# Kernel optimization log

Hardware: AMD Instinct MI355X
Metric: run time of the kernel (lower is better)

## Reference

```python
import jax, jax.numpy as jnp
import numpy as np

BIT, ROW, COL = 4, 8, 8
Y_ROW, Z_COL, K = 128, 128, 256  # inter_dimension = 256, K8 = 32
K8 = K // 8
BATCH, SEQ = 8, 2048


def _unpack_bits(packed, n_bits):
    """Unpack uint8 along last axis, big-endian (MSB first), matching np.packbits."""
    shifts = jnp.arange(7, -1, -1, dtype=jnp.uint8)
    bits = (packed[..., None] >> shifts) & jnp.uint8(1)  # [..., k8, 8]
    return bits.reshape(*packed.shape[:-1], -1)[..., :n_bits]


def setup_inputs() -> dict:
    rng = np.random.default_rng(0)
    # Generate underlying binary tensors so Y_sum / Z_sum are consistent with packed bits.
    Yb = rng.integers(0, 2, size=(BIT, ROW, COL, Y_ROW, K), dtype=np.uint8)
    Zb = rng.integers(0, 2, size=(BIT, ROW, COL, K, Z_COL), dtype=np.uint8)
    Y_packed = np.packbits(Yb, axis=-1)                                # [BIT,ROW,COL,Y_ROW,K8]
    Z_packed = np.packbits(Zb.transpose(0, 1, 2, 4, 3), axis=-1)        # [BIT,ROW,COL,Z_COL,K8]
    Y_sum = Yb.sum(axis=-1, keepdims=True).astype(np.int32)             # [BIT,ROW,COL,Y_ROW,1]
    Z_sum = Zb.sum(axis=-2, keepdims=True).astype(np.int32)             # [BIT,ROW,COL,1,Z_COL]

    key = jax.random.key(0)
    k1, k2, k3, k4, k5, k6 = jax.random.split(key, 6)
    X = jax.random.normal(k1, (BATCH, SEQ, COL * Z_COL), dtype=jnp.float32)
    a = jax.random.normal(k2, (BIT, 1, 1, 1, 1), dtype=jnp.float32) * 0.1
    b = jax.random.normal(k3, (BIT, 1, 1, 1, 1), dtype=jnp.float32) * 0.1
    c = jax.random.normal(k4, (BIT, 1, 1, 1, 1), dtype=jnp.float32) * 0.1
    d = jax.random.normal(k5, (1, 1, 1, 1), dtype=jnp.float32) * 0.1
    bias = jax.random.normal(k6, (ROW * Y_ROW,), dtype=jnp.float32) * 0.1
    return {
        "X": X,
        "Y_packed": jnp.asarray(Y_packed),
        "Z_packed": jnp.asarray(Z_packed),
        "Y_sum": jnp.asarray(Y_sum),
        "Z_sum": jnp.asarray(Z_sum),
        "a": a, "b": b, "c": c, "d": d, "bias": bias,
    }


def reference(X, Y_packed, Z_packed, Y_sum, Z_sum, a, b, c, d, bias):
    dtype = X.dtype
    # Unpack bits (fallback path of _matmul_via_unpack) and do binary matmul.
    Y = _unpack_bits(Y_packed, K).astype(dtype)        # [BIT,ROW,COL,Y_ROW,K]
    Zt = _unpack_bits(Z_packed, K).astype(dtype)       # [BIT,ROW,COL,Z_COL,K]
    W_core = jnp.einsum('brcyk,brczk->brcyz', Y, Zt)   # [BIT,ROW,COL,Y_ROW,Z_COL]
    # Affine recombination over bit planes.
    W = a * W_core + b * Y_sum.astype(dtype) + c * Z_sum.astype(dtype)
    W = W.sum(axis=0) + d                               # [ROW,COL,Y_ROW,Z_COL]
    W = W.transpose(0, 2, 1, 3).reshape(ROW * Y_ROW, COL * Z_COL)
    return X @ W.T + bias
```

## Files before the change

kernel.cpp:

```cpp
#include <hip/hip_runtime.h>
#include <hip/hip_bf16.h>
#include <stdint.h>

typedef unsigned int u32;
typedef unsigned short u16;
typedef __attribute__((ext_vector_type(8))) short short8;
typedef __attribute__((ext_vector_type(4))) float floatx4;

#define N_DIM 1024
#define K_DIM 1024
#define M_DIM 16384
#define EPW  68

__device__ __forceinline__ u32 pack4(uint4 v) {
    return (v.x & 0xffu) | ((v.y & 0xffu) << 8) | ((v.z & 0xffu) << 16) | (v.w << 24);
}

__device__ __forceinline__ u16 bf16rne(float f) {
    u32 u = __float_as_uint(f);
    return (u16)((u + 0x7fffu + ((u >> 16) & 1u)) >> 16);
}

__device__ __forceinline__ void load16_lds(const void* g, void* l) {
    __builtin_amdgcn_global_load_lds(
        (const __attribute__((address_space(1))) void*)g,
        (__attribute__((address_space(3))) void*)l, 16, 0, 0);
}

__global__ __launch_bounds__(256) void build_w(
        const u32* __restrict__ yp, const u32* __restrict__ zp,
        const int* __restrict__ ysum, const int* __restrict__ zsum,
        const float* __restrict__ pa, const float* __restrict__ pb,
        const float* __restrict__ pc, const float* __restrict__ pd,
        __hip_bfloat16* __restrict__ Wb) {
    __shared__ u32 sY[4096];
    __shared__ u32 sZ[1024];
    __shared__ int sYs[512];
    __shared__ int sZs[128];

    const int tid = threadIdx.x;
    const int rc = blockIdx.x >> 2;
    const int zq = blockIdx.x & 3;
    const int r = rc >> 3, c = rc & 7;
    const int z0 = zq * 32;

    const uint4 d0 = ((const uint4*)yp)[0], d1 = ((const uint4*)yp)[1];
    const int sdet = __popc(d0.x) + __popc(d0.y) + __popc(d0.z) + __popc(d0.w)
                   + __popc(d1.x) + __popc(d1.y) + __popc(d1.z) + __popc(d1.w);
    const bool widened = (sdet != ysum[0]);

    if (!widened) {
#pragma unroll
        for (int j = 0; j < 4; ++j) {
            const int chunk = tid + j * 256;
            const int f = chunk * 4;
            const int bit = f >> 10, rem = f & 1023;
            const u32 gw = (u32)((bit * 64 + r * 8 + c) * 1024 + rem);
            ((uint4*)sY)[chunk] = *(const uint4*)(yp + gw);
        }
        {
            const int f = tid * 4;
            const int bit = f >> 8;
            const u32 gw = (u32)((bit * 64 + r * 8 + c) * 1024 + z0 * 8 + (f & 255));
            ((uint4*)sZ)[tid] = *(const uint4*)(zp + gw);
        }
    } else {
#pragma unroll
        for (int j = 0; j < 4; ++j) {
            const int chunk = tid + j * 256;
            const int f = chunk * 4;
            const int bit = f >> 10, rem = f & 1023;
            const u32 gw = (u32)((bit * 64 + r * 8 + c) * 1024 + rem);
            uint4 o;
            o.x = pack4(((const uint4*)yp)[gw + 0]);
            o.y = pack4(((const uint4*)yp)[gw + 1]);
            o.z = pack4(((const uint4*)yp)[gw + 2]);
            o.w = pack4(((const uint4*)yp)[gw + 3]);
            ((uint4*)sY)[chunk] = o;
        }
        {
            const int f = tid * 4;
            const int bit = f >> 8;
            const u32 gw = (u32)((bit * 64 + r * 8 + c) * 1024 + z0 * 8 + (f & 255));
            uint4 o;
            o.x = pack4(((const uint4*)zp)[gw + 0]);
            o.y = pack4(((const uint4*)zp)[gw + 1]);
            o.z = pack4(((const uint4*)zp)[gw + 2]);
            o.w = pack4(((const uint4*)zp)[gw + 3]);
            ((uint4*)sZ)[tid] = o;
        }
    }
    for (int j = tid; j < 512; j += 256) {
        const int bit = j >> 7, y = j & 127;
        sYs[j] = ysum[((bit * 8 + r) * 8 + c) * 128 + y];
    }
    if (tid < 128) {
        const int bit = tid >> 5, zl = tid & 31;
        sZs[tid] = zsum[((bit * 8 + r) * 8 + c) * 128 + z0 + zl];
    }
    __syncthreads();

    float av[4], bv[4], cv[4];
#pragma unroll
    for (int bit = 0; bit < 4; ++bit) { av[bit] = pa[bit]; bv[bit] = pb[bit]; cv[bit] = pc[bit]; }
    const float dv = pd[0];

    const int y = tid & 127;
    const int zh = tid >> 7;

    u32 yw[4][8];
    float base = dv;
#pragma unroll
    for (int bit = 0; bit < 4; ++bit) {
        const uint4 q0 = ((const uint4*)sY)[bit * 256 + y * 2];
        const uint4 q1 = ((const uint4*)sY)[bit * 256 + y * 2 + 1];
        yw[bit][0] = q0.x; yw[bit][1] = q0.y; yw[bit][2] = q0.z; yw[bit][3] = q0.w;
        yw[bit][4] = q1.x; yw[bit][5] = q1.y; yw[bit][6] = q1.z; yw[bit][7] = q1.w;
        base += bv[bit] * (float)sYs[bit * 128 + y];
    }

    const int m = r * 128 + y;
#pragma unroll
    for (int zl2 = 0; zl2 < 16; ++zl2) {
        const int zl = zh * 16 + zl2;
        float wv = base;
#pragma unroll
        for (int bit = 0; bit < 4; ++bit) {
            const uint4 zw0 = ((const uint4*)sZ)[bit * 64 + zl * 2];
            const uint4 zw1 = ((const uint4*)sZ)[bit * 64 + zl * 2 + 1];
            int p = 0;
            p += __popc(yw[bit][0] & zw0.x);
            p += __popc(yw[bit][1] & zw0.y);
            p += __popc(yw[bit][2] & zw0.z);
            p += __popc(yw[bit][3] & zw0.w);
            p += __popc(yw[bit][4] & zw1.x);
            p += __popc(yw[bit][5] & zw1.y);
            p += __popc(yw[bit][6] & zw1.z);
            p += __popc(yw[bit][7] & zw1.w);
            wv += av[bit] * (float)p + cv[bit] * (float)sZs[bit * 32 + zl];
        }
        const int k = c * 128 + z0 + zl;
        Wb[(size_t)m * K_DIM + k] = __float2bfloat16(wv);
    }
}

__global__ __launch_bounds__(256) void convert_x(const float4* __restrict__ X,
                                                 ushort4* __restrict__ Xb) {
    const size_t base = (size_t)blockIdx.x * 512;
    const int tid = threadIdx.x;
    const float4 a = X[base + tid];
    const float4 b = X[base + 256 + tid];
    ushort4 oa, ob;
    oa.x = bf16rne(a.x); oa.y = bf16rne(a.y); oa.z = bf16rne(a.z); oa.w = bf16rne(a.w);
    ob.x = bf16rne(b.x); ob.y = bf16rne(b.y); ob.z = bf16rne(b.z); ob.w = bf16rne(b.w);
    Xb[base + tid] = oa;
    Xb[base + 256 + tid] = ob;
}

__global__ __launch_bounds__(512, 4) void gemm_bias(
        const u16* __restrict__ Xb, const u16* __restrict__ Wb,
        const float* __restrict__ bias, float* __restrict__ out) {
    __shared__ char lds[49152];
    char* As = lds;
    char* Bs = lds + 32768;

    const int tid = threadIdx.x;
    const int lane = tid & 63;
    const int w = tid >> 6;
    const int wr = w >> 1;
    const int wc = w & 1;
    const int mtile = blockIdx.x;
    const int ntile = blockIdx.y;
    const int m0 = mtile * 256, n0 = ntile * 128;

    const int lrow = lane >> 3;
    const int lkc  = (lane & 7) ^ lrow;
    const int fm = lane & 15, fq = lane >> 4;
    const int cx0 = ((0 + fq) ^ (fm & 7)) * 16;
    const int cx1 = ((4 + fq) ^ (fm & 7)) * 16;

    floatx4 acc[4][4] = {};

    for (int kt = 0; kt < K_DIM / 64; ++kt) {
        __syncthreads();
#pragma unroll
        for (int j = 0; j < 4; ++j) {
            const int cw = j * 8 + w;
            const int row = cw * 8 + lrow;
            load16_lds(Xb + (size_t)(m0 + row) * K_DIM + kt * 64 + lkc * 8,
                       As + cw * 1024 + lane * 16);
        }
#pragma unroll
        for (int j = 0; j < 2; ++j) {
            const int cw = j * 8 + w;
            const int row = cw * 8 + lrow;
            load16_lds(Wb + (size_t)(n0 + row) * K_DIM + kt * 64 + lkc * 8,
                       Bs + cw * 1024 + lane * 16);
        }
        __syncthreads();

#pragma unroll
        for (int kk = 0; kk < 2; ++kk) {
            const int cx = kk ? cx1 : cx0;
            short8 afr[4], bfr[4];
#pragma unroll
            for (int mi = 0; mi < 4; ++mi)
                afr[mi] = *(const short8*)(As + (wr * 64 + mi * 16 + fm) * 128 + cx);
#pragma unroll
            for (int ni = 0; ni < 4; ++ni)
                bfr[ni] = *(const short8*)(Bs + (wc * 64 + ni * 16 + fm) * 128 + cx);
#pragma unroll
            for (int mi = 0; mi < 4; ++mi)
#pragma unroll
                for (int ni = 0; ni < 4; ++ni)
                    acc[mi][ni] = __builtin_amdgcn_mfma_f32_16x16x32_bf16(
                        afr[mi], bfr[ni], acc[mi][ni], 0, 0, 0);
        }
    }

    float bias_r[4];
#pragma unroll
    for (int ni = 0; ni < 4; ++ni)
        bias_r[ni] = bias[n0 + wc * 64 + ni * 16 + fm];

    __syncthreads();
    float* ep = (float*)lds + w * (16 * EPW);
    const int gm0 = m0 + wr * 64;
    const int gn0 = n0 + wc * 64;

#pragma unroll
    for (int mi = 0; mi < 4; ++mi) {
#pragma unroll
        for (int ni = 0; ni < 4; ++ni)
#pragma unroll
            for (int reg = 0; reg < 4; ++reg)
                ep[(fq * 4 + reg) * EPW + ni * 16 + fm] = acc[mi][ni][reg] + bias_r[ni];
#pragma unroll
        for (int t = 0; t < 4; ++t) {
            const int lr = t * 4 + fq;
            const float4 v = *(const float4*)(ep + lr * EPW + fm * 4);
            *(float4*)(out + (size_t)(gm0 + mi * 16 + lr) * N_DIM + gn0 + fm * 4) = v;
        }
    }
}

extern "C" void kernel_launch(void* const* d_in, const int* in_sizes, int n_in,
                              void* d_out, int out_size, void* d_ws, size_t ws_size,
                              hipStream_t stream) {
    const float* X   = (const float*)d_in[0];
    const u32*   Yp  = (const u32*)d_in[1];
    const u32*   Zp  = (const u32*)d_in[2];
    const int*   Ys  = (const int*)d_in[3];
    const int*   Zs  = (const int*)d_in[4];
    const float* pa  = (const float*)d_in[5];
    const float* pb  = (const float*)d_in[6];
    const float* pc  = (const float*)d_in[7];
    const float* pd  = (const float*)d_in[8];
    const float* bias = (const float*)d_in[9];
    float* out = (float*)d_out;

    char* ws = (char*)d_ws;
    __hip_bfloat16* Wb = (__hip_bfloat16*)ws;
    u16*            Xb = (u16*)(ws + (2u << 20));

    build_w<<<256, 256, 0, stream>>>(Yp, Zp, Ys, Zs, pa, pb, pc, pd, Wb);
    convert_x<<<8192, 256, 0, stream>>>((const float4*)X, (ushort4*)Xb);
    gemm_bias<<<dim3(64, 8), 512, 0, stream>>>(Xb, (const u16*)Wb, bias, out);
}
```

Measured before the change: 171.3 us.

## Switch GEMM to 32x32x16 MFMA with 128x128 tiles and 256-thread blocks

Replaces the 16x16x32 bf16 MFMA with the 32x32x16 variant, giving each wave a 64x64 sub-tile as 2x2 32x32 fragments. The block tile shrinks from 256x128 with 8 waves to 128x128 with 4 waves, which doubles the grid and reduces LDS per block. The epilogue is rewritten for the 32x32 accumulator layout. This cuts LDS fragment reads per FLOP and may improve occupancy, but loses some A-tile reuse per block.

```diff
diff --git a/kernel.cpp b/kernel.cpp
--- a/kernel.cpp
+++ b/kernel.cpp
@@ -5,12 +5,12 @@
 typedef unsigned int u32;
 typedef unsigned short u16;
 typedef __attribute__((ext_vector_type(8))) short short8;
-typedef __attribute__((ext_vector_type(4))) float floatx4;
+typedef __attribute__((ext_vector_type(16))) float floatx16;
 
 #define N_DIM 1024
 #define K_DIM 1024
 #define M_DIM 16384
-#define EPW  68
+#define EPW2 68
 
 __device__ __forceinline__ u32 pack4(uint4 v) {
     return (v.x & 0xffu) | ((v.y & 0xffu) << 8) | ((v.z & 0xffu) << 16) | (v.w << 24);
@@ -157,12 +157,12 @@
     Xb[base + 256 + tid] = ob;
 }
 
-__global__ __launch_bounds__(512, 4) void gemm_bias(
+__global__ __launch_bounds__(256, 4) void gemm_bias(
         const u16* __restrict__ Xb, const u16* __restrict__ Wb,
         const float* __restrict__ bias, float* __restrict__ out) {
-    __shared__ char lds[49152];
+    __shared__ __align__(16) char lds[34816];
     char* As = lds;
-    char* Bs = lds + 32768;
+    char* Bs = lds + 16384;
 
     const int tid = threadIdx.x;
     const int lane = tid & 63;
@@ -171,28 +171,27 @@
     const int wc = w & 1;
     const int mtile = blockIdx.x;
     const int ntile = blockIdx.y;
-    const int m0 = mtile * 256, n0 = ntile * 128;
+    const int m0 = mtile * 128, n0 = ntile * 128;
 
     const int lrow = lane >> 3;
     const int lkc  = (lane & 7) ^ lrow;
-    const int fm = lane & 15, fq = lane >> 4;
-    const int cx0 = ((0 + fq) ^ (fm & 7)) * 16;
-    const int cx1 = ((4 + fq) ^ (fm & 7)) * 16;
-
-    floatx4 acc[4][4] = {};
+    const int fn = lane & 31;
+    const int fh = lane >> 5;
+
+    floatx16 acc[2][2] = {};
 
     for (int kt = 0; kt < K_DIM / 64; ++kt) {
         __syncthreads();
 #pragma unroll
         for (int j = 0; j < 4; ++j) {
-            const int cw = j * 8 + w;
+            const int cw = j * 4 + w;
             const int row = cw * 8 + lrow;
             load16_lds(Xb + (size_t)(m0 + row) * K_DIM + kt * 64 + lkc * 8,
                        As + cw * 1024 + lane * 16);
         }
 #pragma unroll
-        for (int j = 0; j < 2; ++j) {
-            const int cw = j * 8 + w;
+        for (int j = 0; j < 4; ++j) {
+            const int cw = j * 4 + w;
             const int row = cw * 8 + lrow;
             load16_lds(Wb + (size_t)(n0 + row) * K_DIM + kt * 64 + lkc * 8,
                        Bs + cw * 1024 + lane * 16);
@@ -200,46 +199,54 @@
         __syncthreads();
 
 #pragma unroll
-        for (int kk = 0; kk < 2; ++kk) {
-            const int cx = kk ? cx1 : cx0;
-            short8 afr[4], bfr[4];
-#pragma unroll
-            for (int mi = 0; mi < 4; ++mi)
-                afr[mi] = *(const short8*)(As + (wr * 64 + mi * 16 + fm) * 128 + cx);
-#pragma unroll
-            for (int ni = 0; ni < 4; ++ni)
-                bfr[ni] = *(const short8*)(Bs + (wc * 64 + ni * 16 + fm) * 128 + cx);
-#pragma unroll
-            for (int mi = 0; mi < 4; ++mi)
-#pragma unroll
-                for (int ni = 0; ni < 4; ++ni)
-                    acc[mi][ni] = __builtin_amdgcn_mfma_f32_16x16x32_bf16(
-                        afr[mi], bfr[ni], acc[mi][ni], 0, 0, 0);
-        }
-    }
-
-    float bias_r[4];
-#pragma unroll
-    for (int ni = 0; ni < 4; ++ni)
-        bias_r[ni] = bias[n0 + wc * 64 + ni * 16 + fm];
+        for (int ks = 0; ks < 4; ++ks) {
+            const int chunk = ks * 2 + fh;
+            short8 af[2], bf[2];
+#pragma unroll
+            for (int mi = 0; mi < 2; ++mi) {
+                const int row = wr * 64 + mi * 32 + fn;
+                af[mi] = *(const short8*)(As + row * 128 + ((chunk ^ (row & 7)) * 16));
+            }
+#pragma unroll
+            for (int ni = 0; ni < 2; ++ni) {
+                const int row = wc * 64 + ni * 32 + fn;
+                bf[ni] = *(const short8*)(Bs + row * 128 + ((chunk ^ (row & 7)) * 16));
+            }
+#pragma unroll
+            for (int mi = 0; mi < 2; ++mi)
+#pragma unroll
+                for (int ni = 0; ni < 2; ++ni)
+                    acc[mi][ni] = __builtin_amdgcn_mfma_f32_32x32x16_bf16(
+                        af[mi], bf[ni], acc[mi][ni], 0, 0, 0);
+        }
+    }
+
+    float bias_r[2];
+#pragma unroll
+    for (int ni = 0; ni < 2; ++ni)
+        bias_r[ni] = bias[n0 + wc * 64 + ni * 32 + fn];
 
     __syncthreads();
-    float* ep = (float*)lds + w * (16 * EPW);
+    float* ep = (float*)lds + w * (32 * EPW2);
     const int gm0 = m0 + wr * 64;
     const int gn0 = n0 + wc * 64;
 
 #pragma unroll
-    for (int mi = 0; mi < 4; ++mi) {
-#pragma unroll
-        for (int ni = 0; ni < 4; ++ni)
-#pragma unroll
-            for (int reg = 0; reg < 4; ++reg)
-                ep[(fq * 4 + reg) * EPW + ni * 16 + fm] = acc[mi][ni][reg] + bias_r[ni];
-#pragma unroll
-        for (int t = 0; t < 4; ++t) {
-            const int lr = t * 4 + fq;
-            const float4 v = *(const float4*)(ep + lr * EPW + fm * 4);
-            *(float4*)(out + (size_t)(gm0 + mi * 16 + lr) * N_DIM + gn0 + fm * 4) = v;
+    for (int mi = 0; mi < 2; ++mi) {
+#pragma unroll
+        for (int ni = 0; ni < 2; ++ni)
+#pragma unroll
+            for (int reg = 0; reg < 16; ++reg) {
+                const int rl = (reg & 3) + 8 * (reg >> 2) + 4 * fh;
+                ep[rl * EPW2 + ni * 32 + fn] = acc[mi][ni][reg] + bias_r[ni];
+            }
+#pragma unroll
+        for (int t = 0; t < 8; ++t) {
+            const int flat = t * 64 + lane;
+            const int lr = flat >> 4;
+            const int c4 = flat & 15;
+            const float4 v = *(const float4*)(ep + lr * EPW2 + c4 * 4);
+            *(float4*)(out + (size_t)(gm0 + mi * 32 + lr) * N_DIM + gn0 + c4 * 4) = v;
         }
     }
 }
@@ -265,5 +272,5 @@
 
     build_w<<<256, 256, 0, stream>>>(Yp, Zp, Ys, Zs, pa, pb, pc, pd, Wb);
     convert_x<<<8192, 256, 0, stream>>>((const float4*)X, (ushort4*)Xb);
-    gemm_bias<<<dim3(64, 8), 512, 0, stream>>>(Xb, (const u16*)Wb, bias, out);
-}
+    gemm_bias<<<dim3(128, 8), 256, 0, stream>>>(Xb, (const u16*)Wb, bias, out);
+}
```

After: 182.2 us. 6.4% more time.
